# Optimization experiments

Measured on AMD Instinct MI355X. Metric: run time of the kernel, lower is better.

## Reference

```python
import jax, jax.numpy as jnp
import numpy as np

D = 256          # out_feats
H = 4            # n_heads
DH = D // H      # per-head feats
S = 8192         # number of snapshots (segments)
PER = 32         # edges (selected papers) per snapshot
E = S * PER      # total edges
NP = 200000      # number of papers
ST = 10          # snapshot_types (embedding has ST+1 rows, padding_idx=-1)
SLOPE = 0.01     # LeakyReLU negative slope (torch default)


def setup_inputs() -> dict:
    key = jax.random.key(0)
    ks = jax.random.split(key, 20)
    sc = 1.0 / np.sqrt(D)
    papers = jax.random.normal(ks[0], (NP, D), dtype=jnp.float32)
    snapshots = jax.random.normal(ks[1], (S, D), dtype=jnp.float32)
    cur_snapshot_types = jax.random.randint(ks[2], (S,), 0, ST + 1, dtype=jnp.int32)
    is_cite = jax.random.randint(ks[3], (NP,), 0, 2, dtype=jnp.int32)
    selected_indicator = jax.random.randint(ks[4], (E,), 0, NP, dtype=jnp.int64)
    # contiguous sorted segment ids, PER edges per snapshot (matches valid_num_nodes)
    index = jnp.repeat(jnp.arange(S, dtype=jnp.int32), PER)
    # linear layers (torch Linear: y = x @ W.T + b)
    W_src = jax.random.normal(ks[5], (D, D), dtype=jnp.float32) * sc
    b_src = jnp.zeros((D,), dtype=jnp.float32)
    W_dst = jax.random.normal(ks[6], (D, D), dtype=jnp.float32) * sc
    b_dst = jnp.zeros((D,), dtype=jnp.float32)
    W_out = jax.random.normal(ks[7], (D, D), dtype=jnp.float32) * sc
    b_out = jnp.zeros((D,), dtype=jnp.float32)
    # node attr embeddings (2 rows, padding_idx=0 -> row 0 zero)
    emb_cite = jax.random.normal(ks[8], (2, D), dtype=jnp.float32).at[0].set(0.0)
    emb_ref = jax.random.normal(ks[9], (2, D), dtype=jnp.float32).at[0].set(0.0)
    emb_target = jax.random.normal(ks[10], (2, D), dtype=jnp.float32).at[0].set(0.0)
    # snapshot type embedding (ST+1 rows, padding_idx=-1 -> last row zero)
    snapshot_emb = jax.random.normal(ks[11], (ST + 1, D), dtype=jnp.float32).at[-1].set(0.0)
    # attention vectors, xavier_normal with relu gain
    gain = np.sqrt(2.0)
    std = gain * np.sqrt(2.0 / (H * DH + 1))
    attn = jax.random.normal(ks[12], (1, H, DH), dtype=jnp.float32) * std
    attn_t = jax.random.normal(ks[13], (1, H, DH), dtype=jnp.float32) * std
    return {
        "papers": papers, "snapshots": snapshots,
        "W_src": W_src, "b_src": b_src, "W_dst": W_dst, "b_dst": b_dst,
        "W_out": W_out, "b_out": b_out,
        "emb_cite": emb_cite, "emb_ref": emb_ref, "emb_target": emb_target,
        "snapshot_emb": snapshot_emb, "attn": attn, "attn_t": attn_t,
        "cur_snapshot_types": cur_snapshot_types, "is_cite": is_cite,
        "selected_indicator": selected_indicator, "index": index,
    }


def _leaky(x):
    return jnp.where(x >= 0, x, SLOPE * x)


def reference(papers, snapshots, W_src, b_src, W_dst, b_dst, W_out, b_out,
              emb_cite, emb_ref, emb_target, snapshot_emb, attn, attn_t,
              cur_snapshot_types, is_cite, selected_indicator, index):
    # gather src papers per edge: [E, D]
    h_src = papers[selected_indicator]
    feat_src = (h_src @ W_src.T + b_src).reshape(-1, H, DH)          # [E,H,DH]
    ic = is_cite[selected_indicator]
    # original uses 'is_cite' indices for all three attr embeddings (faithful)
    src_type_h = (emb_cite[ic] + emb_ref[ic] + emb_target[ic]).reshape(-1, H, DH)
    dst_type_h = snapshot_emb[cur_snapshot_types].reshape(-1, H, DH)  # [S,H,DH]
    feat_dst = (snapshots @ W_dst.T + b_dst).reshape(-1, H, DH)[index]  # [E,H,DH]
    # per-edge attention logits
    e = (_leaky(feat_src + feat_dst) * attn).sum(axis=-1)             # [E,H]
    et = (_leaky(src_type_h + dst_type_h[index]) * attn_t).sum(axis=-1)
    e = e + et
    # segment (edge) softmax over destination snapshots
    m = jax.lax.stop_gradient(jax.ops.segment_max(e, index, num_segments=S))
    ex = jnp.exp(e - m[index])
    den = jax.ops.segment_sum(ex, index, num_segments=S)
    a = (ex / den[index])[..., None]                                  # [E,H,1]
    # weighted segment-sum aggregation
    x = feat_src * a
    sum_out = jax.ops.segment_sum(x, index, num_segments=S).reshape(S, D)
    return sum_out @ W_out.T + b_out
```

## Files before the change

### kernel.cpp

```cpp
#include <hip/hip_runtime.h>
#include <hip/hip_fp16.h>
#include <type_traits>

#define NSNAP 8192
#define PER 32
#define SLOPE 0.01f

using half8   = __attribute__((ext_vector_type(8))) _Float16;
using floatx4 = __attribute__((ext_vector_type(4))) float;

__device__ __forceinline__ float leaky(float x) { return x >= 0.f ? x : SLOPE * x; }

__device__ __forceinline__ unsigned pack2(float a, float b) {
    __half2 h = __floats2half2_rn(a, b);
    return *reinterpret_cast<unsigned*>(&h);
}

template <typename AT, typename OT, bool DO_PACK>
__global__ __launch_bounds__(256) void gemm64(const AT* __restrict__ A,
                                              const float* __restrict__ W,
                                              const float* __restrict__ bias,
                                              OT* __restrict__ Cout, int M,
                                              const float* __restrict__ Wsrc,
                                              _Float16* __restrict__ Wh) {
    if constexpr (DO_PACK) {
        if (blockIdx.y == 4) {
            if (blockIdx.x < 32) {
                const int t = blockIdx.x * 256 + threadIdx.x;
                const int lane = t & 63;
                const int wj = (t >> 6) & 15;
                const int k0 = t >> 10;
                const int n = (wj >> 2) * 64 + (wj & 3) * 16 + (lane & 15);
                const int k = k0 * 32 + (lane >> 4) * 8;
                const float4 v0 = *(const float4*)(Wsrc + (long)n * 256 + k);
                const float4 v1 = *(const float4*)(Wsrc + (long)n * 256 + k + 4);
                *(uint4*)(Wh + (long)t * 8) = make_uint4(pack2(v0.x, v0.y), pack2(v0.z, v0.w),
                                                         pack2(v1.x, v1.y), pack2(v1.z, v1.w));
            }
            return;
        }
    }
    constexpr int LDA = 40;
    __shared__ _Float16 Asl[64 * LDA];
    __shared__ _Float16 Wsl[64 * LDA];

    const int m0 = blockIdx.x * 64;
    const int n0 = blockIdx.y * 64;
    const int tid = threadIdx.x;
    const int lane = tid & 63;
    const int wave = tid >> 6;
    const int wm = (wave & 1) * 32;
    const int wn = (wave >> 1) * 32;
    const int l15 = lane & 15;
    const int quad = lane >> 4;

    floatx4 acc[2][2];
#pragma unroll
    for (int i = 0; i < 2; i++)
#pragma unroll
        for (int j = 0; j < 2; j++) acc[i][j] = (floatx4)0.f;

    for (int k0 = 0; k0 < 256; k0 += 32) {
        __syncthreads();
#pragma unroll
        for (int it = 0; it < 2; ++it) {
            const int idx = tid + it * 256;
            const int row = idx >> 3;
            const int c4 = idx & 7;
            if constexpr (std::is_same_v<AT, float>) {
                const float4 v = *(const float4*)(A + (long)(m0 + row) * 256 + k0 + c4 * 4);
                *(uint2*)(&Asl[row * LDA + c4 * 4]) = make_uint2(pack2(v.x, v.y), pack2(v.z, v.w));
            } else {
                const uint2 v = *(const uint2*)(A + (long)(m0 + row) * 256 + k0 + c4 * 4);
                *(uint2*)(&Asl[row * LDA + c4 * 4]) = v;
            }
            const float4 w = *(const float4*)(W + (long)(n0 + row) * 256 + k0 + c4 * 4);
            *(uint2*)(&Wsl[row * LDA + c4 * 4]) = make_uint2(pack2(w.x, w.y), pack2(w.z, w.w));
        }
        __syncthreads();

        half8 af[2], bf[2];
#pragma unroll
        for (int i = 0; i < 2; i++)
            af[i] = *reinterpret_cast<const half8*>(&Asl[(wm + i * 16 + l15) * LDA + quad * 8]);
#pragma unroll
        for (int j = 0; j < 2; j++)
            bf[j] = *reinterpret_cast<const half8*>(&Wsl[(wn + j * 16 + l15) * LDA + quad * 8]);
#pragma unroll
        for (int i = 0; i < 2; i++)
#pragma unroll
            for (int j = 0; j < 2; j++)
                acc[i][j] = __builtin_amdgcn_mfma_f32_16x16x32_f16(af[i], bf[j], acc[i][j], 0, 0, 0);
    }

#pragma unroll
    for (int j = 0; j < 2; j++) {
        const int gcol = n0 + wn + j * 16 + l15;
        const float bv = bias[gcol];
#pragma unroll
        for (int i = 0; i < 2; i++) {
            const int rbase = m0 + wm + i * 16 + quad * 4;
#pragma unroll
            for (int r = 0; r < 4; r++) {
                const float v = acc[i][j][r] + bv;
                if constexpr (std::is_same_v<OT, __half>)
                    Cout[(long)(rbase + r) * 256 + gcol] = __float2half(v);
                else
                    Cout[(long)(rbase + r) * 256 + gcol] = v;
            }
        }
    }
}

__global__ __launch_bounds__(256, 4) void fused_attn(
    const float* __restrict__ papers, const _Float16* __restrict__ Wh,
    const float* __restrict__ b_src, const float* __restrict__ F,
    const float* __restrict__ emb_cite, const float* __restrict__ emb_ref,
    const float* __restrict__ emb_target, const float* __restrict__ snap_emb,
    const float* __restrict__ attn, const float* __restrict__ attn_t,
    const int* __restrict__ types, const int* __restrict__ is_cite,
    const int* __restrict__ sel, __half* __restrict__ SO) {
    __shared__ _Float16 Asl[64 * 256];
    __shared__ int ic_l[64];

    const int tid = threadIdx.x;
    const int lane = tid & 63;
    const int wave = tid >> 6;
    const int l15 = lane & 15;
    const int quad = lane >> 4;
    const int sbase = blockIdx.x * 2;
    const int ebase = blockIdx.x * 64;

    if (tid < 64) ic_l[tid] = is_cite[sel[ebase + tid]];

    {
        const int row = wave * 16 + l15;
        const long arow = (long)sel[ebase + row];
        const float* src = papers + arow * 256;
#pragma unroll
        for (int m = 0; m < 16; m++) {
            const float4 v = *(const float4*)(src + m * 16 + quad * 4);
            const int c8 = m * 2 + (quad >> 1);
            const int slot = (c8 >> 2) * 256 + wave * 64 + (c8 & 3) * 16 + l15;
            *(uint2*)(&Asl[slot * 8 + (quad & 1) * 4]) =
                make_uint2(pack2(v.x, v.y), pack2(v.z, v.w));
        }
    }
    __syncthreads();

    floatx4 acc[4][4];
#pragma unroll
    for (int i = 0; i < 4; i++)
#pragma unroll
        for (int j = 0; j < 4; j++) acc[i][j] = (floatx4)0.f;

    for (int k0 = 0; k0 < 8; k0++) {
        half8 af[4], bf[4];
#pragma unroll
        for (int i = 0; i < 4; i++)
            af[i] = *reinterpret_cast<const half8*>(&Asl[(k0 * 256 + i * 64 + lane) * 8]);
#pragma unroll
        for (int j = 0; j < 4; j++)
            bf[j] = *reinterpret_cast<const half8*>(Wh + ((k0 * 16 + wave * 4 + j) * 64 + lane) * 8);
#pragma unroll
        for (int i = 0; i < 4; i++)
#pragma unroll
            for (int j = 0; j < 4; j++)
                acc[i][j] = __builtin_amdgcn_mfma_f32_16x16x32_f16(af[i], bf[j], acc[i][j], 0, 0, 0);
    }

    float bsrc_j[4], attn_j[4], F0_j[4], F1_j[4];
#pragma unroll
    for (int j = 0; j < 4; j++) {
        const int col = 64 * wave + j * 16 + l15;
        bsrc_j[j] = b_src[col];
        attn_j[j] = attn[col];
        F0_j[j] = F[(long)sbase * 256 + col];
        F1_j[j] = F[(long)(sbase + 1) * 256 + col];
    }
#pragma unroll
    for (int i = 0; i < 4; i++)
#pragma unroll
        for (int j = 0; j < 4; j++)
#pragma unroll
            for (int r = 0; r < 4; r++) acc[i][j][r] += bsrc_j[j];

    const int D = 64 * wave + lane;
    const float at_d = attn_t[D];
    const float src0 = emb_cite[D] + emb_ref[D] + emb_target[D];
    const float src1 = emb_cite[256 + D] + emb_ref[256 + D] + emb_target[256 + D];
    float et[2][2];
#pragma unroll
    for (int sn = 0; sn < 2; sn++) {
        const float dstt = snap_emb[types[sbase + sn] * 256 + D];
        float p0 = leaky(src0 + dstt) * at_d;
        float p1 = leaky(src1 + dstt) * at_d;
#pragma unroll
        for (int off = 32; off; off >>= 1) {
            p0 += __shfl_xor(p0, off);
            p1 += __shfl_xor(p1, off);
        }
        et[sn][0] = p0;
        et[sn][1] = p1;
    }

    float lg[4][4];
#pragma unroll
    for (int i = 0; i < 4; i++) {
        const int sn = i >> 1;
#pragma unroll
        for (int r = 0; r < 4; r++) {
            float p = 0.f;
#pragma unroll
            for (int j = 0; j < 4; j++)
                p += leaky(acc[i][j][r] + (sn == 0 ? F0_j[j] : F1_j[j])) * attn_j[j];
#pragma unroll
            for (int off = 1; off <= 8; off <<= 1) p += __shfl_xor(p, off);
            const int row = i * 16 + quad * 4 + r;
            lg[i][r] = p + et[sn][ic_l[row]];
        }
    }

    float aw[4][4];
#pragma unroll
    for (int sn = 0; sn < 2; sn++) {
        float m = -3.4e38f;
#pragma unroll
        for (int ii = 0; ii < 2; ii++)
#pragma unroll
            for (int r = 0; r < 4; r++) m = fmaxf(m, lg[sn * 2 + ii][r]);
        m = fmaxf(m, __shfl_xor(m, 16));
        m = fmaxf(m, __shfl_xor(m, 32));
        float den = 0.f;
#pragma unroll
        for (int ii = 0; ii < 2; ii++)
#pragma unroll
            for (int r = 0; r < 4; r++) {
                const float ex = __expf(lg[sn * 2 + ii][r] - m);
                aw[sn * 2 + ii][r] = ex;
                den += ex;
            }
        den += __shfl_xor(den, 16);
        den += __shfl_xor(den, 32);
        const float inv = 1.f / den;
#pragma unroll
        for (int ii = 0; ii < 2; ii++)
#pragma unroll
            for (int r = 0; r < 4; r++) aw[sn * 2 + ii][r] *= inv;
    }

#pragma unroll
    for (int sn = 0; sn < 2; sn++) {
#pragma unroll
        for (int j = 0; j < 4; j++) {
            float o = 0.f;
#pragma unroll
            for (int ii = 0; ii < 2; ii++)
#pragma unroll
                for (int r = 0; r < 4; r++) o += aw[sn * 2 + ii][r] * acc[sn * 2 + ii][j][r];
            o += __shfl_xor(o, 16);
            o += __shfl_xor(o, 32);
            if (quad == sn)
                SO[(long)(sbase + sn) * 256 + 64 * wave + j * 16 + l15] = __float2half(o);
        }
    }
}

extern "C" void kernel_launch(void* const* d_in, const int* in_sizes, int n_in,
                              void* d_out, int out_size, void* d_ws, size_t ws_size,
                              hipStream_t stream) {
    const float* papers     = (const float*)d_in[0];
    const float* snapshots  = (const float*)d_in[1];
    const float* W_src      = (const float*)d_in[2];
    const float* b_src      = (const float*)d_in[3];
    const float* W_dst      = (const float*)d_in[4];
    const float* b_dst      = (const float*)d_in[5];
    const float* W_out      = (const float*)d_in[6];
    const float* b_out      = (const float*)d_in[7];
    const float* emb_cite   = (const float*)d_in[8];
    const float* emb_ref    = (const float*)d_in[9];
    const float* emb_target = (const float*)d_in[10];
    const float* snap_emb   = (const float*)d_in[11];
    const float* attn       = (const float*)d_in[12];
    const float* attn_t     = (const float*)d_in[13];
    const int* types        = (const int*)d_in[14];
    const int* is_cite      = (const int*)d_in[15];
    const int* sel          = (const int*)d_in[16];

    char* ws = (char*)d_ws;
    float*     F    = (float*)ws;
    __half*    SO   = (__half*)(ws + 8388608);
    _Float16*  Wh   = (_Float16*)(ws + 12582912);

    gemm64<float, float, true><<<dim3(128, 5), 256, 0, stream>>>(snapshots, W_dst, b_dst, F,
                                                                 NSNAP, W_src, Wh);
    fused_attn<<<NSNAP / 2, 256, 0, stream>>>(papers, Wh, b_src, F, emb_cite, emb_ref,
                                              emb_target, snap_emb, attn, attn_t, types,
                                              is_cite, sel, SO);
    gemm64<__half, float, false><<<dim3(128, 4), 256, 0, stream>>>(SO, W_out, b_out,
                                                                   (float*)d_out, NSNAP,
                                                                   nullptr, nullptr);
}
```

Before: 382.9 us.

## Software-pipeline MFMA operand loads and hoist small gathers before barrier

Moves the small parameter and embedding gathers ahead of the shared-memory barrier so their latency overlaps the paper-row staging. Replaces the shared is_cite array with a wave ballot mask, and double-buffers the A and W fragment loads across k-steps of the MFMA loop. Raises the launch-bounds occupancy hint from 4 to 5 blocks per CU. The extra prefetch registers may conflict with the tighter register budget and cause spills.

```diff
diff --git a/kernel.cpp b/kernel.cpp
--- a/kernel.cpp
+++ b/kernel.cpp
@@ -112,7 +112,7 @@
     }
 }
 
-__global__ __launch_bounds__(256, 4) void fused_attn(
+__global__ __launch_bounds__(256, 5) void fused_attn(
     const float* __restrict__ papers, const _Float16* __restrict__ Wh,
     const float* __restrict__ b_src, const float* __restrict__ F,
     const float* __restrict__ emb_cite, const float* __restrict__ emb_ref,
@@ -121,7 +121,6 @@
     const int* __restrict__ types, const int* __restrict__ is_cite,
     const int* __restrict__ sel, __half* __restrict__ SO) {
     __shared__ _Float16 Asl[64 * 256];
-    __shared__ int ic_l[64];
 
     const int tid = threadIdx.x;
     const int lane = tid & 63;
@@ -131,8 +130,6 @@
     const int sbase = blockIdx.x * 2;
     const int ebase = blockIdx.x * 64;
 
-    if (tid < 64) ic_l[tid] = is_cite[sel[ebase + tid]];
-
     {
         const int row = wave * 16 + l15;
         const long arow = (long)sel[ebase + row];
@@ -146,28 +143,6 @@
                 make_uint2(pack2(v.x, v.y), pack2(v.z, v.w));
         }
     }
-    __syncthreads();
-
-    floatx4 acc[4][4];
-#pragma unroll
-    for (int i = 0; i < 4; i++)
-#pragma unroll
-        for (int j = 0; j < 4; j++) acc[i][j] = (floatx4)0.f;
-
-    for (int k0 = 0; k0 < 8; k0++) {
-        half8 af[4], bf[4];
-#pragma unroll
-        for (int i = 0; i < 4; i++)
-            af[i] = *reinterpret_cast<const half8*>(&Asl[(k0 * 256 + i * 64 + lane) * 8]);
-#pragma unroll
-        for (int j = 0; j < 4; j++)
-            bf[j] = *reinterpret_cast<const half8*>(Wh + ((k0 * 16 + wave * 4 + j) * 64 + lane) * 8);
-#pragma unroll
-        for (int i = 0; i < 4; i++)
-#pragma unroll
-            for (int j = 0; j < 4; j++)
-                acc[i][j] = __builtin_amdgcn_mfma_f32_16x16x32_f16(af[i], bf[j], acc[i][j], 0, 0, 0);
-    }
 
     float bsrc_j[4], attn_j[4], F0_j[4], F1_j[4];
 #pragma unroll
@@ -178,23 +153,70 @@
         F0_j[j] = F[(long)sbase * 256 + col];
         F1_j[j] = F[(long)(sbase + 1) * 256 + col];
     }
+    const int Dd = 64 * wave + lane;
+    const float at_d = attn_t[Dd];
+    const float src0 = emb_cite[Dd] + emb_ref[Dd] + emb_target[Dd];
+    const float src1 = emb_cite[256 + Dd] + emb_ref[256 + Dd] + emb_target[256 + Dd];
+    float dstt[2];
+    dstt[0] = snap_emb[types[sbase] * 256 + Dd];
+    dstt[1] = snap_emb[types[sbase + 1] * 256 + Dd];
+    const int icv = is_cite[sel[ebase + lane]];
+    const unsigned long long icmask = __ballot(icv != 0);
+    half8 bf_cur[4], bf_nxt[4];
+#pragma unroll
+    for (int j = 0; j < 4; j++)
+        bf_cur[j] = *reinterpret_cast<const half8*>(Wh + ((wave * 4 + j) * 64 + lane) * 8);
+
+    __syncthreads();
+
+    floatx4 acc[4][4];
 #pragma unroll
     for (int i = 0; i < 4; i++)
 #pragma unroll
+        for (int j = 0; j < 4; j++) acc[i][j] = (floatx4)0.f;
+
+    half8 af_cur[4], af_nxt[4];
+#pragma unroll
+    for (int i = 0; i < 4; i++)
+        af_cur[i] = *reinterpret_cast<const half8*>(&Asl[(i * 64 + lane) * 8]);
+#pragma unroll
+    for (int k0 = 0; k0 < 8; k0++) {
+        if (k0 < 7) {
+#pragma unroll
+            for (int j = 0; j < 4; j++)
+                bf_nxt[j] = *reinterpret_cast<const half8*>(
+                    Wh + (((k0 + 1) * 16 + wave * 4 + j) * 64 + lane) * 8);
+#pragma unroll
+            for (int i = 0; i < 4; i++)
+                af_nxt[i] =
+                    *reinterpret_cast<const half8*>(&Asl[((k0 + 1) * 256 + i * 64 + lane) * 8]);
+        }
+#pragma unroll
+        for (int i = 0; i < 4; i++)
+#pragma unroll
+            for (int j = 0; j < 4; j++)
+                acc[i][j] =
+                    __builtin_amdgcn_mfma_f32_16x16x32_f16(af_cur[i], bf_cur[j], acc[i][j], 0, 0, 0);
+        if (k0 < 7) {
+#pragma unroll
+            for (int i = 0; i < 4; i++) af_cur[i] = af_nxt[i];
+#pragma unroll
+            for (int j = 0; j < 4; j++) bf_cur[j] = bf_nxt[j];
+        }
+    }
+
+#pragma unroll
+    for (int i = 0; i < 4; i++)
+#pragma unroll
         for (int j = 0; j < 4; j++)
 #pragma unroll
             for (int r = 0; r < 4; r++) acc[i][j][r] += bsrc_j[j];
 
-    const int D = 64 * wave + lane;
-    const float at_d = attn_t[D];
-    const float src0 = emb_cite[D] + emb_ref[D] + emb_target[D];
-    const float src1 = emb_cite[256 + D] + emb_ref[256 + D] + emb_target[256 + D];
     float et[2][2];
 #pragma unroll
     for (int sn = 0; sn < 2; sn++) {
-        const float dstt = snap_emb[types[sbase + sn] * 256 + D];
-        float p0 = leaky(src0 + dstt) * at_d;
-        float p1 = leaky(src1 + dstt) * at_d;
+        float p0 = leaky(src0 + dstt[sn]) * at_d;
+        float p1 = leaky(src1 + dstt[sn]) * at_d;
 #pragma unroll
         for (int off = 32; off; off >>= 1) {
             p0 += __shfl_xor(p0, off);
@@ -217,7 +239,7 @@
 #pragma unroll
             for (int off = 1; off <= 8; off <<= 1) p += __shfl_xor(p, off);
             const int row = i * 16 + quad * 4 + r;
-            lg[i][r] = p + et[sn][ic_l[row]];
+            lg[i][r] = p + ((icmask >> row) & 1ull ? et[sn][1] : et[sn][0]);
         }
     }
 
```

Result: slower. 492.3 us (+28.6%).
